# Kernel optimization log

Measured on AMD Instinct MI355X. Metric: run time of the kernel, lower is better.

## Reference

```python
import jax, jax.numpy as jnp
import numpy as np

B, L, H, E = 4, 2048, 8, 64
S, D = L, E  # causal mask forces L == S


def setup_inputs() -> dict:
    key = jax.random.key(0)
    kq, kk, kv, km = jax.random.split(key, 4)
    return {
        "queries": jax.random.normal(kq, (B, L, H, E), dtype=jnp.float32),
        "keys": jax.random.normal(kk, (B, S, H, E), dtype=jnp.float32),
        "values": jax.random.normal(kv, (B, S, H, D), dtype=jnp.float32),
        "map": jax.random.normal(km, (S, S), dtype=jnp.float32),
    }


def reference(queries, keys, values, map):
    # queries: [B,L,H,E], keys: [B,S,H,E], values: [B,S,H,D], map: [S,S]
    E_ = queries.shape[-1]
    scale = 1.0 / jnp.sqrt(jnp.asarray(E_, dtype=queries.dtype))
    # raw attention scores: [B,H,L,S]
    scores = jnp.einsum("blhe,bshe->bhls", queries, keys)
    # mix scores with learned map along the key axis: [B,H,L,S]
    scores = jnp.einsum("bhls,st->bhlt", scores, map)
    # causal mask (TriangularCausalMask: triu with diagonal=1 is masked)
    Lq = queries.shape[1]
    causal = jnp.triu(jnp.ones((Lq, Lq), dtype=bool), k=1)  # [L,S]
    scores = jnp.where(causal[None, None, :, :], -jnp.inf, scores)
    attn = jax.nn.softmax(scale * scores, axis=-1)  # dropout p=0.0 -> identity
    out = jnp.einsum("bhls,bshd->blhd", attn, values)  # [B,L,H,D]
    return out
```

## Files before the change

kernel.cpp:

```cpp
#include <hip/hip_runtime.h>


typedef short bf16x8 __attribute__((ext_vector_type(8)));
typedef float f32x4 __attribute__((ext_vector_type(4)));
typedef float f32x16 __attribute__((ext_vector_type(16)));
typedef unsigned short u16x8 __attribute__((ext_vector_type(8)));
typedef unsigned int u32x4 __attribute__((ext_vector_type(4)));

typedef __attribute__((address_space(1))) const void gvoid;
typedef __attribute__((address_space(3))) void lvoid;

__device__ __forceinline__ unsigned short f2bf(float x) {
  unsigned int u = __float_as_uint(x);
  u += 0x7FFFu + ((u >> 16) & 1u);
  return (unsigned short)(u >> 16);
}
__device__ __forceinline__ float bf2f(unsigned short h) {
  return __uint_as_float(((unsigned int)h) << 16);
}
__device__ __forceinline__ unsigned int cvtpk(float lo, float hi) {
  unsigned int r;
  asm("v_cvt_pk_bf16_f32 %0, %1, %2" : "=v"(r) : "v"(lo), "v"(hi));
  return r;
}

__device__ __forceinline__ void gload16(const unsigned short* g, unsigned short* l) {
  __builtin_amdgcn_global_load_lds((gvoid*)g, (lvoid*)l, 16, 0, 0);
}

template <int NW>
__device__ __forceinline__ void stage_tile(const unsigned short* __restrict__ g,
                                           int gstride, unsigned short* l,
                                           int rows, int tid) {
  const int lane = tid & 63, w = tid >> 6;
  const int nch = rows << 3;
  for (int c0 = (w << 6); c0 < nch; c0 += NW * 64) {
    const int c = c0 + lane;
    const int row = c >> 3;
    const int bir = (c & 7) << 4;
    const int sb = bir ^ ((row & 7) << 4);
    gload16(g + (size_t)row * gstride + (sb >> 1), l + (size_t)c0 * 8);
  }
}

__device__ __forceinline__ int swz(int row, int byteInRow) {
  return row * 128 + (byteInRow ^ ((row & 7) << 4));
}

__global__ __launch_bounds__(256) void prep_m(const float* __restrict__ M,
                                              unsigned short* __restrict__ Mh,
                                              unsigned short* __restrict__ Ml) {
  __shared__ float Ts[64][68];
  const int s0 = blockIdx.x << 6, t0 = blockIdx.y << 6;
  const int tid = threadIdx.x, r = tid >> 2, c0 = (tid & 3) << 4;
  const float* src = M + (size_t)(s0 + r) * 2048 + t0 + c0;
#pragma unroll
  for (int j = 0; j < 4; ++j)
    *(float4*)&Ts[r][c0 + 4 * j] = *(const float4*)(src + 4 * j);
  __syncthreads();
  u16x8 h0, h1, l0v, l1v;
#pragma unroll
  for (int j = 0; j < 8; ++j) {
    float x = Ts[c0 + j][r];
    unsigned short hh = f2bf(x);
    h0[j] = hh; l0v[j] = f2bf(x - bf2f(hh));
  }
#pragma unroll
  for (int j = 8; j < 16; ++j) {
    float x = Ts[c0 + j][r];
    unsigned short hh = f2bf(x);
    h1[j - 8] = hh; l1v[j - 8] = f2bf(x - bf2f(hh));
  }
  const size_t o = (size_t)(t0 + r) * 2048 + s0 + c0;
  *(u16x8*)(Mh + o) = h0; *(u16x8*)(Mh + o + 8) = h1;
  *(u16x8*)(Ml + o) = l0v; *(u16x8*)(Ml + o + 8) = l1v;
}

__global__ __launch_bounds__(256) void prep_kv(const float* __restrict__ src4d,
                                               unsigned short* __restrict__ Dh,
                                               unsigned short* __restrict__ Dl,
                                               int has_lo) {
  __shared__ float Ts[64][68];
  const int s0 = blockIdx.x << 6, bh = blockIdx.y;
  const int b = bh >> 3, h = bh & 7;
  const int tid = threadIdx.x, r = tid >> 2, c0 = (tid & 3) << 4;
  const float* src = src4d + ((size_t)(b * 2048 + s0 + r) * 8 + h) * 64 + c0;
#pragma unroll
  for (int j = 0; j < 4; ++j)
    *(float4*)&Ts[r][c0 + 4 * j] = *(const float4*)(src + 4 * j);
  __syncthreads();
  u16x8 h0, h1, l0v, l1v;
#pragma unroll
  for (int j = 0; j < 8; ++j) {
    float x = Ts[c0 + j][r];
    unsigned short hh = f2bf(x);
    h0[j] = hh; l0v[j] = f2bf(x - bf2f(hh));
  }
#pragma unroll
  for (int j = 8; j < 16; ++j) {
    float x = Ts[c0 + j][r];
    unsigned short hh = f2bf(x);
    h1[j - 8] = hh; l1v[j - 8] = f2bf(x - bf2f(hh));
  }
  const size_t o = ((size_t)bh * 64 + r) * 2048 + s0 + c0;
  *(u16x8*)(Dh + o) = h0; *(u16x8*)(Dh + o + 8) = h1;
  if (has_lo) { *(u16x8*)(Dl + o) = l0v; *(u16x8*)(Dl + o + 8) = l1v; }
}

__global__ __launch_bounds__(256) void km_mfma(
    const unsigned short* __restrict__ Mth, const unsigned short* __restrict__ Mtl,
    const unsigned short* __restrict__ Kth, const unsigned short* __restrict__ Ktl,
    unsigned short* __restrict__ KMh, unsigned short* __restrict__ KMl) {
  __shared__ __attribute__((aligned(16))) unsigned short sm[24576];
  unsigned short* MtH = sm;
  unsigned short* MtL = sm + 8192;
  unsigned short* KtH = sm + 16384;
  unsigned short* KtL = sm + 20480;
  const int tid = threadIdx.x, lane = tid & 63, w = tid >> 6;
  const int g = lane >> 4, li = lane & 15;
  const int t0 = blockIdx.x << 7;
  const int bh = blockIdx.y;
  const unsigned short* KtHb = Kth + (size_t)bh * 64 * 2048;
  const unsigned short* KtLb = Ktl + (size_t)bh * 64 * 2048;

  f32x4 acc[2][4];
#pragma unroll
  for (int mi = 0; mi < 2; ++mi)
#pragma unroll
    for (int ni = 0; ni < 4; ++ni) acc[mi][ni] = (f32x4){0.f, 0.f, 0.f, 0.f};

  for (int s0 = 0; s0 < 2048; s0 += 64) {
    __syncthreads();
    stage_tile<4>(Mth + (size_t)t0 * 2048 + s0, 2048, MtH, 128, tid);
    stage_tile<4>(Mtl + (size_t)t0 * 2048 + s0, 2048, MtL, 128, tid);
    stage_tile<4>(KtHb + s0, 2048, KtH, 64, tid);
    stage_tile<4>(KtLb + s0, 2048, KtL, 64, tid);
    asm volatile("s_waitcnt vmcnt(0)" ::: "memory");
    __syncthreads();
#pragma unroll
    for (int kk = 0; kk < 2; ++kk) {
      const int kb = (kk * 32 + 8 * g) * 2;
      bf16x8 aH[2], aL[2];
#pragma unroll
      for (int mi = 0; mi < 2; ++mi) {
        const int row = (w << 5) + (mi << 4) + li;
        aH[mi] = *(const bf16x8*)((const char*)MtH + swz(row, kb));
        aL[mi] = *(const bf16x8*)((const char*)MtL + swz(row, kb));
      }
#pragma unroll
      for (int ni = 0; ni < 4; ++ni) {
        const int row = (ni << 4) + li;
        const int off = swz(row, kb);
        const bf16x8 bH = *(const bf16x8*)((const char*)KtH + off);
        const bf16x8 bL = *(const bf16x8*)((const char*)KtL + off);
#pragma unroll
        for (int mi = 0; mi < 2; ++mi) {
          acc[mi][ni] = __builtin_amdgcn_mfma_f32_16x16x32_bf16(aH[mi], bH, acc[mi][ni], 0, 0, 0);
          acc[mi][ni] = __builtin_amdgcn_mfma_f32_16x16x32_bf16(aH[mi], bL, acc[mi][ni], 0, 0, 0);
          acc[mi][ni] = __builtin_amdgcn_mfma_f32_16x16x32_bf16(aL[mi], bH, acc[mi][ni], 0, 0, 0);
        }
      }
    }
  }
  const size_t base = (size_t)bh * 2048 * 64;
#pragma unroll
  for (int mi = 0; mi < 2; ++mi)
#pragma unroll
    for (int r = 0; r < 4; ++r) {
      const int trow = t0 + (w << 5) + (mi << 4) + (g << 2) + r;
#pragma unroll
      for (int ni = 0; ni < 4; ++ni) {
        const float x = acc[mi][ni][r];
        const unsigned short hh = f2bf(x);
        const size_t idx = base + (size_t)trow * 64 + (ni << 4) + li;
        KMh[idx] = hh;
        KMl[idx] = f2bf(x - bf2f(hh));
      }
    }
}

__global__ __launch_bounds__(256, 3) void attn32(
    const float* __restrict__ Q, const unsigned short* __restrict__ KMh,
    const unsigned short* __restrict__ KMl, const unsigned short* __restrict__ Vt,
    float* __restrict__ Out, float* __restrict__ Opart, float* __restrict__ Ml) {
  __shared__ __attribute__((aligned(16))) unsigned short sm[24576];
  const int tid = threadIdx.x, lane = tid & 63, w = tid >> 6;
  const int g2 = lane >> 5, li5 = lane & 31;

  const int bid = (int)blockIdx.x;
  const int x = bid & 7, n = bid >> 3;
  const int slot = n >> 5, j = n & 31;
  const int bh = (x << 2) | (j & 3);
  const int kk = j >> 2;
  int lt, jt0, jtEnd;
  bool partial;
  if (slot == 2) {
    lt = kk; jt0 = 0; jtEnd = 2 * kk + 1; partial = false;
  } else {
    lt = 15 - kk;
    const int half = 16 - kk;
    jt0 = slot * half; jtEnd = jt0 + half - 1; partial = true;
  }
  const int b = bh >> 3, h = bh & 7;
  const int l0 = lt << 7;
  const int qg = l0 + (w << 5) + li5;
  const int rloc = (w << 5) + li5;

  const float SC2 = 0.18033688011112042f;
  bf16x8 qh[4], ql[4];
  {
    const float* qsrc = Q + (((size_t)(b * 2048 + qg) * 8 + h) << 6) + (g2 << 3);
#pragma unroll
    for (int kki = 0; kki < 4; ++kki) {
      const float4 v0 = *(const float4*)(qsrc + 16 * kki);
      const float4 v1 = *(const float4*)(qsrc + 16 * kki + 4);
      const float xs[8] = {v0.x, v0.y, v0.z, v0.w, v1.x, v1.y, v1.z, v1.w};
#pragma unroll
      for (int jj = 0; jj < 8; ++jj) {
        const float xv = xs[jj] * SC2;
        const unsigned short hh = f2bf(xv);
        qh[kki][jj] = (short)hh;
        ql[kki][jj] = (short)f2bf(xv - bf2f(hh));
      }
    }
  }

  f32x16 o0 = {0,0,0,0,0,0,0,0,0,0,0,0,0,0,0,0};
  f32x16 o1 = {0,0,0,0,0,0,0,0,0,0,0,0,0,0,0,0};
  f32x16 lsacc = {0,0,0,0,0,0,0,0,0,0,0,0,0,0,0,0};
  float m2 = -1e30f;
  bf16x8 ones;
#pragma unroll
  for (int jj = 0; jj < 8; ++jj) ones[jj] = (short)0x3F80;

  const unsigned short* KHb = KMh + (size_t)bh * 2048 * 64;
  const unsigned short* KLb = KMl + (size_t)bh * 2048 * 64;
  const unsigned short* VTb = Vt + (size_t)bh * 64 * 2048;

  const int jtmax_w = 2 * lt + (w >> 1);

  {
    unsigned short* s0b = sm + (jt0 & 1) * 12288;
    stage_tile<4>(KHb + (size_t)jt0 * 4096, 64, s0b, 64, tid);
    stage_tile<4>(KLb + (size_t)jt0 * 4096, 64, s0b + 4096, 64, tid);
    stage_tile<4>(VTb + jt0 * 64, 2048, s0b + 8192, 64, tid);
  }
  asm volatile("s_waitcnt vmcnt(0)" ::: "memory");
  __builtin_amdgcn_s_barrier();
  __builtin_amdgcn_sched_barrier(0);

  for (int jt = jt0; jt <= jtEnd; ++jt) {
    const int cur = jt & 1;
    if (jt < jtEnd) {
      unsigned short* nb = sm + (cur ^ 1) * 12288;
      stage_tile<4>(KHb + (size_t)(jt + 1) * 4096, 64, nb, 64, tid);
      stage_tile<4>(KLb + (size_t)(jt + 1) * 4096, 64, nb + 4096, 64, tid);
      stage_tile<4>(VTb + (jt + 1) * 64, 2048, nb + 8192, 64, tid);
    }

    if (jt <= jtmax_w) {
      const unsigned short* KH = sm + cur * 12288;
      const unsigned short* KL = KH + 4096;
      const unsigned short* VT = KH + 8192;

      f32x16 z0 = {0,0,0,0,0,0,0,0,0,0,0,0,0,0,0,0};
      f32x16 z1 = {0,0,0,0,0,0,0,0,0,0,0,0,0,0,0,0};
      __builtin_amdgcn_s_setprio(1);
#pragma unroll
      for (int kki = 0; kki < 4; ++kki) {
        const int cb = 32 * kki + 16 * g2;
        const bf16x8 a0h = *(const bf16x8*)((const char*)KH + swz(li5, cb));
        const bf16x8 a0l = *(const bf16x8*)((const char*)KL + swz(li5, cb));
        const bf16x8 a1h = *(const bf16x8*)((const char*)KH + swz(32 + li5, cb));
        const bf16x8 a1l = *(const bf16x8*)((const char*)KL + swz(32 + li5, cb));
        z0 = __builtin_amdgcn_mfma_f32_32x32x16_bf16(a0h, qh[kki], z0, 0, 0, 0);
        z0 = __builtin_amdgcn_mfma_f32_32x32x16_bf16(a0h, ql[kki], z0, 0, 0, 0);
        z0 = __builtin_amdgcn_mfma_f32_32x32x16_bf16(a0l, qh[kki], z0, 0, 0, 0);
        z1 = __builtin_amdgcn_mfma_f32_32x32x16_bf16(a1h, qh[kki], z1, 0, 0, 0);
        z1 = __builtin_amdgcn_mfma_f32_32x32x16_bf16(a1h, ql[kki], z1, 0, 0, 0);
        z1 = __builtin_amdgcn_mfma_f32_32x32x16_bf16(a1l, qh[kki], z1, 0, 0, 0);
      }
      __builtin_amdgcn_s_setprio(0);

      const bool needmask = (jt * 64 + 63 > l0 + (w << 5));
      if (needmask) {
        const int thr = qg - jt * 64;
#pragma unroll
        for (int rr = 0; rr < 16; ++rr) {
          const int tl = (g2 << 2) + ((rr >> 2) << 3) + (rr & 3);
          if (tl > thr) z0[rr] = -1e30f;
          if (tl + 32 > thr) z1[rr] = -1e30f;
        }
      }

      float t16[16];
#pragma unroll
      for (int rr = 0; rr < 16; ++rr) t16[rr] = fmaxf(z0[rr], z1[rr]);
#pragma unroll
      for (int s = 8; s; s >>= 1)
#pragma unroll
        for (int rr = 0; rr < 8; ++rr)
          if (rr < s) t16[rr] = fmaxf(t16[rr], t16[rr + s]);
      const float mx = fmaxf(t16[0], __shfl_xor(t16[0], 32));
      if (__any(mx > m2 + 11.0f)) {
        const float m2n = fmaxf(m2, mx);
        const float fs = exp2f(m2 - m2n);
        m2 = m2n;
#pragma unroll
        for (int rr = 0; rr < 16; ++rr) { o0[rr] *= fs; o1[rr] *= fs; }
        lsacc[0] *= fs;
      }

      float pv0[16], pv1[16];
#pragma unroll
      for (int rr = 0; rr < 16; ++rr) {
        pv0[rr] = exp2f(z0[rr] - m2);
        pv1[rr] = exp2f(z1[rr] - m2);
      }
      unsigned int W0[8], W1[8];
#pragma unroll
      for (int i = 0; i < 8; ++i) {
        W0[i] = cvtpk(pv0[2 * i], pv0[2 * i + 1]);
        W1[i] = cvtpk(pv1[2 * i], pv1[2 * i + 1]);
      }
      asm volatile("v_permlane32_swap_b32 %0, %1" : "+v"(W0[0]), "+v"(W0[2]));
      asm volatile("v_permlane32_swap_b32 %0, %1" : "+v"(W0[1]), "+v"(W0[3]));
      asm volatile("v_permlane32_swap_b32 %0, %1" : "+v"(W0[4]), "+v"(W0[6]));
      asm volatile("v_permlane32_swap_b32 %0, %1" : "+v"(W0[5]), "+v"(W0[7]));
      asm volatile("v_permlane32_swap_b32 %0, %1" : "+v"(W1[0]), "+v"(W1[2]));
      asm volatile("v_permlane32_swap_b32 %0, %1" : "+v"(W1[1]), "+v"(W1[3]));
      asm volatile("v_permlane32_swap_b32 %0, %1" : "+v"(W1[4]), "+v"(W1[6]));
      asm volatile("v_permlane32_swap_b32 %0, %1" : "+v"(W1[5]), "+v"(W1[7]));
      bf16x8 pf[4];
      {
        u32x4 f0 = {W0[0], W0[1], W0[2], W0[3]};
        u32x4 f1 = {W0[4], W0[5], W0[6], W0[7]};
        u32x4 f2 = {W1[0], W1[1], W1[2], W1[3]};
        u32x4 f3 = {W1[4], W1[5], W1[6], W1[7]};
        pf[0] = __builtin_bit_cast(bf16x8, f0);
        pf[1] = __builtin_bit_cast(bf16x8, f1);
        pf[2] = __builtin_bit_cast(bf16x8, f2);
        pf[3] = __builtin_bit_cast(bf16x8, f3);
      }

      __builtin_amdgcn_s_setprio(1);
#pragma unroll
      for (int kki = 0; kki < 4; ++kki) {
        const int cb = 32 * kki + 16 * g2;
        const bf16x8 v0f = *(const bf16x8*)((const char*)VT + swz(li5, cb));
        const bf16x8 v1f = *(const bf16x8*)((const char*)VT + swz(32 + li5, cb));
        o0 = __builtin_amdgcn_mfma_f32_32x32x16_bf16(v0f, pf[kki], o0, 0, 0, 0);
        o1 = __builtin_amdgcn_mfma_f32_32x32x16_bf16(v1f, pf[kki], o1, 0, 0, 0);
        lsacc = __builtin_amdgcn_mfma_f32_32x32x16_bf16(ones, pf[kki], lsacc, 0, 0, 0);
      }
      __builtin_amdgcn_s_setprio(0);
    }

    asm volatile("s_waitcnt vmcnt(0)" ::: "memory");
    __builtin_amdgcn_s_barrier();
    __builtin_amdgcn_sched_barrier(0);
  }

  if (!partial) {
    const float inv = 1.f / lsacc[0];
    float* ob = Out + (((size_t)(b * 2048 + qg) * 8 + h) << 6);
#pragma unroll
    for (int r2 = 0; r2 < 4; ++r2) {
      const int doff = (g2 << 2) + (r2 << 3);
      float4 s0 = make_float4(o0[4 * r2] * inv, o0[4 * r2 + 1] * inv,
                              o0[4 * r2 + 2] * inv, o0[4 * r2 + 3] * inv);
      *(float4*)(ob + doff) = s0;
      float4 s1 = make_float4(o1[4 * r2] * inv, o1[4 * r2 + 1] * inv,
                              o1[4 * r2 + 2] * inv, o1[4 * r2 + 3] * inv);
      *(float4*)(ob + 32 + doff) = s1;
    }
  } else {
    const size_t pidx = (((size_t)slot * 32 + bh) * 8 + kk) * 128 + rloc;
    float* op = Opart + pidx * 64;
#pragma unroll
    for (int r2 = 0; r2 < 4; ++r2) {
      const int doff = (g2 << 2) + (r2 << 3);
      *(float4*)(op + doff) =
          make_float4(o0[4 * r2], o0[4 * r2 + 1], o0[4 * r2 + 2], o0[4 * r2 + 3]);
      *(float4*)(op + 32 + doff) =
          make_float4(o1[4 * r2], o1[4 * r2 + 1], o1[4 * r2 + 2], o1[4 * r2 + 3]);
    }
    Ml[pidx * 2] = m2;
    Ml[pidx * 2 + 1] = lsacc[0];
  }
}

__global__ __launch_bounds__(256) void attn_combine(
    const float* __restrict__ Opart, const float* __restrict__ Ml,
    float* __restrict__ Out) {
  const int tid = threadIdx.x;
  const int rowg = (int)blockIdx.x * 32 + (tid >> 3);
  const int d0 = (tid & 7) << 3;
  const int r = rowg & 127, kk = (rowg >> 7) & 7, bh = rowg >> 10;
  const int b = bh >> 3, h = bh & 7;
  const int lt = 15 - kk;
  const size_t pidx = (((size_t)bh * 8 + kk) * 128 + r);
  const size_t PSLOT = (size_t)32 * 8 * 128 * 64;
  const size_t MSLOT = (size_t)32 * 8 * 128 * 2;
  const float m0 = Ml[pidx * 2], ls0 = Ml[pidx * 2 + 1];
  const float m1 = Ml[MSLOT + pidx * 2], ls1 = Ml[MSLOT + pidx * 2 + 1];
  const float mm = fmaxf(m0, m1);
  const float w0 = exp2f(m0 - mm), w1 = exp2f(m1 - mm);
  const float inv = 1.f / (ls0 * w0 + ls1 * w1);
  const float* p0 = Opart + pidx * 64 + d0;
  const float* p1 = Opart + PSLOT + pidx * 64 + d0;
  const float4 a0 = *(const float4*)(p0);
  const float4 a1 = *(const float4*)(p0 + 4);
  const float4 b0 = *(const float4*)(p1);
  const float4 b1 = *(const float4*)(p1 + 4);
  const int qg = lt * 128 + r;
  float* o = Out + (((size_t)(b * 2048 + qg) * 8 + h) << 6) + d0;
  *(float4*)o = make_float4((a0.x * w0 + b0.x * w1) * inv,
                            (a0.y * w0 + b0.y * w1) * inv,
                            (a0.z * w0 + b0.z * w1) * inv,
                            (a0.w * w0 + b0.w * w1) * inv);
  *(float4*)(o + 4) = make_float4((a1.x * w0 + b1.x * w1) * inv,
                                  (a1.y * w0 + b1.y * w1) * inv,
                                  (a1.z * w0 + b1.z * w1) * inv,
                                  (a1.w * w0 + b1.w * w1) * inv);
}

extern "C" void kernel_launch(void* const* d_in, const int* in_sizes, int n_in,
                              void* d_out, int out_size, void* d_ws, size_t ws_size,
                              hipStream_t stream) {
  const float* Q = (const float*)d_in[0];
  const float* K = (const float*)d_in[1];
  const float* V = (const float*)d_in[2];
  const float* M = (const float*)d_in[3];
  float* Out = (float*)d_out;
  char* ws = (char*)d_ws;
  const size_t MB = 1u << 20;
  unsigned short* Mth = (unsigned short*)(ws);
  unsigned short* Mtl = (unsigned short*)(ws + 8 * MB);
  unsigned short* Kth = (unsigned short*)(ws + 16 * MB);
  unsigned short* Ktl = (unsigned short*)(ws + 24 * MB);
  unsigned short* Vts = (unsigned short*)(ws + 32 * MB);
  unsigned short* KMh = (unsigned short*)(ws + 40 * MB);
  unsigned short* KMl = (unsigned short*)(ws + 48 * MB);
  float* Opart = (float*)(ws);
  float* Mlp = (float*)(ws + 16 * MB);

  prep_m<<<dim3(32, 32), 256, 0, stream>>>(M, Mth, Mtl);
  prep_kv<<<dim3(32, 32), 256, 0, stream>>>(K, Kth, Ktl, 1);
  prep_kv<<<dim3(32, 32), 256, 0, stream>>>(V, Vts, (unsigned short*)nullptr, 0);
  km_mfma<<<dim3(16, 32), 256, 0, stream>>>(Mth, Mtl, Kth, Ktl, KMh, KMl);
  attn32<<<dim3(768), 256, 0, stream>>>(Q, KMh, KMl, Vts, Out, Opart, Mlp);
  attn_combine<<<dim3(1024), 256, 0, stream>>>(Opart, Mlp, Out);
}
```

Before: 147.9 us.

## Split every query tile in half, single-buffer V, store bf16 partials

Every query tile's key range is now split into two halves across 1024 blocks, replacing the mixed full and partial scheme. All outputs then go through the combine kernel, and the partials are stored as bf16 instead of fp32. V staging uses a single LDS buffer loaded each iteration, with a mid-iteration barrier and vmcnt wait, while K hi/lo stay double-buffered. This shrinks LDS so four blocks fit per CU. The aim is better load balance and occupancy and less partial-output traffic. The cost is an extra barrier per tile, combine work for every row, and bf16 rounding of the partial accumulators.

```diff
diff --git a/kernel.cpp b/kernel.cpp
--- a/kernel.cpp
+++ b/kernel.cpp
@@ -45,6 +45,10 @@
 
 __device__ __forceinline__ int swz(int row, int byteInRow) {
   return row * 128 + (byteInRow ^ ((row & 7) << 4));
+}
+
+__device__ __forceinline__ int chunk_off(int c, int gstride) {
+  return (c >> 3) * gstride + ((((c & 7) ^ ((c >> 3) & 7))) << 3);
 }
 
 __global__ __launch_bounds__(256) void prep_m(const float* __restrict__ M,
@@ -179,11 +183,11 @@
     }
 }
 
-__global__ __launch_bounds__(256, 3) void attn32(
+__global__ __launch_bounds__(256, 4) void attn32(
     const float* __restrict__ Q, const unsigned short* __restrict__ KMh,
     const unsigned short* __restrict__ KMl, const unsigned short* __restrict__ Vt,
-    float* __restrict__ Out, float* __restrict__ Opart, float* __restrict__ Ml) {
-  __shared__ __attribute__((aligned(16))) unsigned short sm[24576];
+    unsigned short* __restrict__ Opart, float* __restrict__ Ml) {
+  __shared__ __attribute__((aligned(16))) unsigned short sm[20480];
   const int tid = threadIdx.x, lane = tid & 63, w = tid >> 6;
   const int g2 = lane >> 5, li5 = lane & 31;
 
@@ -191,20 +195,22 @@
   const int x = bid & 7, n = bid >> 3;
   const int slot = n >> 5, j = n & 31;
   const int bh = (x << 2) | (j & 3);
-  const int kk = j >> 2;
-  int lt, jt0, jtEnd;
-  bool partial;
-  if (slot == 2) {
-    lt = kk; jt0 = 0; jtEnd = 2 * kk + 1; partial = false;
-  } else {
-    lt = 15 - kk;
-    const int half = 16 - kk;
-    jt0 = slot * half; jtEnd = jt0 + half - 1; partial = true;
-  }
+  const int k = j >> 2;
+  const int hf = slot & 1;
+  const int lt = (slot < 2) ? (15 - k) : k;
+  const int half = lt + 1;
+  const int jt0 = hf * half;
+  const int jtEnd = jt0 + half - 1;
   const int b = bh >> 3, h = bh & 7;
   const int l0 = lt << 7;
   const int qg = l0 + (w << 5) + li5;
   const int rloc = (w << 5) + li5;
+
+  const int c0 = tid, c1 = tid + 256;
+  const int ko0 = chunk_off(c0, 64), ko1 = chunk_off(c1, 64);
+  const int vo0 = chunk_off(c0, 2048), vo1 = chunk_off(c1, 2048);
+  const int ld0 = c0 << 3, ld1 = c1 << 3;
+  unsigned short* VTl = sm + 16384;
 
   const float SC2 = 0.18033688011112042f;
   bf16x8 qh[4], ql[4];
@@ -233,35 +239,41 @@
 #pragma unroll
   for (int jj = 0; jj < 8; ++jj) ones[jj] = (short)0x3F80;
 
-  const unsigned short* KHb = KMh + (size_t)bh * 2048 * 64;
-  const unsigned short* KLb = KMl + (size_t)bh * 2048 * 64;
-  const unsigned short* VTb = Vt + (size_t)bh * 64 * 2048;
+  const unsigned short* khsrc = KMh + (size_t)bh * 2048 * 64 + (size_t)jt0 * 4096;
+  const unsigned short* klsrc = KMl + (size_t)bh * 2048 * 64 + (size_t)jt0 * 4096;
+  const unsigned short* vsrc = Vt + (size_t)bh * 64 * 2048 + jt0 * 64;
 
   const int jtmax_w = 2 * lt + (w >> 1);
 
   {
-    unsigned short* s0b = sm + (jt0 & 1) * 12288;
-    stage_tile<4>(KHb + (size_t)jt0 * 4096, 64, s0b, 64, tid);
-    stage_tile<4>(KLb + (size_t)jt0 * 4096, 64, s0b + 4096, 64, tid);
-    stage_tile<4>(VTb + jt0 * 64, 2048, s0b + 8192, 64, tid);
-  }
+    unsigned short* kb = sm + ((jt0 & 1) << 13);
+    gload16(khsrc + ko0, kb + ld0);
+    gload16(khsrc + ko1, kb + ld1);
+    gload16(klsrc + ko0, kb + 4096 + ld0);
+    gload16(klsrc + ko1, kb + 4096 + ld1);
+  }
+  khsrc += 4096; klsrc += 4096;
   asm volatile("s_waitcnt vmcnt(0)" ::: "memory");
   __builtin_amdgcn_s_barrier();
   __builtin_amdgcn_sched_barrier(0);
 
   for (int jt = jt0; jt <= jtEnd; ++jt) {
-    const int cur = jt & 1;
-    if (jt < jtEnd) {
-      unsigned short* nb = sm + (cur ^ 1) * 12288;
-      stage_tile<4>(KHb + (size_t)(jt + 1) * 4096, 64, nb, 64, tid);
-      stage_tile<4>(KLb + (size_t)(jt + 1) * 4096, 64, nb + 4096, 64, tid);
-      stage_tile<4>(VTb + (jt + 1) * 64, 2048, nb + 8192, 64, tid);
-    }
-
-    if (jt <= jtmax_w) {
-      const unsigned short* KH = sm + cur * 12288;
+    gload16(vsrc + vo0, VTl + ld0);
+    gload16(vsrc + vo1, VTl + ld1);
+    {
+      unsigned short* kb = sm + (((jt + 1) & 1) << 13);
+      gload16(khsrc + ko0, kb + ld0);
+      gload16(khsrc + ko1, kb + ld1);
+      gload16(klsrc + ko0, kb + 4096 + ld0);
+      gload16(klsrc + ko1, kb + 4096 + ld1);
+    }
+    khsrc += 4096; klsrc += 4096; vsrc += 64;
+
+    const bool act = (jt <= jtmax_w);
+    bf16x8 pf[4];
+    if (act) {
+      const unsigned short* KH = sm + ((jt & 1) << 13);
       const unsigned short* KL = KH + 4096;
-      const unsigned short* VT = KH + 8192;
 
       f32x16 z0 = {0,0,0,0,0,0,0,0,0,0,0,0,0,0,0,0};
       f32x16 z1 = {0,0,0,0,0,0,0,0,0,0,0,0,0,0,0,0};
@@ -331,7 +343,6 @@
       asm volatile("v_permlane32_swap_b32 %0, %1" : "+v"(W1[1]), "+v"(W1[3]));
       asm volatile("v_permlane32_swap_b32 %0, %1" : "+v"(W1[4]), "+v"(W1[6]));
       asm volatile("v_permlane32_swap_b32 %0, %1" : "+v"(W1[5]), "+v"(W1[7]));
-      bf16x8 pf[4];
       {
         u32x4 f0 = {W0[0], W0[1], W0[2], W0[3]};
         u32x4 f1 = {W0[4], W0[5], W0[6], W0[7]};
@@ -342,13 +353,19 @@
         pf[2] = __builtin_bit_cast(bf16x8, f2);
         pf[3] = __builtin_bit_cast(bf16x8, f3);
       }
-
+    }
+
+    asm volatile("s_waitcnt vmcnt(4)" ::: "memory");
+    __builtin_amdgcn_s_barrier();
+    __builtin_amdgcn_sched_barrier(0);
+
+    if (act) {
       __builtin_amdgcn_s_setprio(1);
 #pragma unroll
       for (int kki = 0; kki < 4; ++kki) {
         const int cb = 32 * kki + 16 * g2;
-        const bf16x8 v0f = *(const bf16x8*)((const char*)VT + swz(li5, cb));
-        const bf16x8 v1f = *(const bf16x8*)((const char*)VT + swz(32 + li5, cb));
+        const bf16x8 v0f = *(const bf16x8*)((const char*)VTl + swz(li5, cb));
+        const bf16x8 v1f = *(const bf16x8*)((const char*)VTl + swz(32 + li5, cb));
         o0 = __builtin_amdgcn_mfma_f32_32x32x16_bf16(v0f, pf[kki], o0, 0, 0, 0);
         o1 = __builtin_amdgcn_mfma_f32_32x32x16_bf16(v1f, pf[kki], o1, 0, 0, 0);
         lsacc = __builtin_amdgcn_mfma_f32_32x32x16_bf16(ones, pf[kki], lsacc, 0, 0, 0);
@@ -361,68 +378,52 @@
     __builtin_amdgcn_sched_barrier(0);
   }
 
-  if (!partial) {
-    const float inv = 1.f / lsacc[0];
-    float* ob = Out + (((size_t)(b * 2048 + qg) * 8 + h) << 6);
-#pragma unroll
-    for (int r2 = 0; r2 < 4; ++r2) {
-      const int doff = (g2 << 2) + (r2 << 3);
-      float4 s0 = make_float4(o0[4 * r2] * inv, o0[4 * r2 + 1] * inv,
-                              o0[4 * r2 + 2] * inv, o0[4 * r2 + 3] * inv);
-      *(float4*)(ob + doff) = s0;
-      float4 s1 = make_float4(o1[4 * r2] * inv, o1[4 * r2 + 1] * inv,
-                              o1[4 * r2 + 2] * inv, o1[4 * r2 + 3] * inv);
-      *(float4*)(ob + 32 + doff) = s1;
-    }
-  } else {
-    const size_t pidx = (((size_t)slot * 32 + bh) * 8 + kk) * 128 + rloc;
-    float* op = Opart + pidx * 64;
-#pragma unroll
-    for (int r2 = 0; r2 < 4; ++r2) {
-      const int doff = (g2 << 2) + (r2 << 3);
-      *(float4*)(op + doff) =
-          make_float4(o0[4 * r2], o0[4 * r2 + 1], o0[4 * r2 + 2], o0[4 * r2 + 3]);
-      *(float4*)(op + 32 + doff) =
-          make_float4(o1[4 * r2], o1[4 * r2 + 1], o1[4 * r2 + 2], o1[4 * r2 + 3]);
-    }
-    Ml[pidx * 2] = m2;
-    Ml[pidx * 2 + 1] = lsacc[0];
-  }
+  const size_t pidx = (((size_t)bh * 16 + lt) << 7) + rloc;
+  unsigned short* op = Opart + (size_t)hf * 4194304 + pidx * 64;
+#pragma unroll
+  for (int r2 = 0; r2 < 4; ++r2) {
+    const int doff = (g2 << 2) + (r2 << 3);
+    uint2 pa, pb;
+    pa.x = cvtpk(o0[4 * r2], o0[4 * r2 + 1]);
+    pa.y = cvtpk(o0[4 * r2 + 2], o0[4 * r2 + 3]);
+    *(uint2*)(op + doff) = pa;
+    pb.x = cvtpk(o1[4 * r2], o1[4 * r2 + 1]);
+    pb.y = cvtpk(o1[4 * r2 + 2], o1[4 * r2 + 3]);
+    *(uint2*)(op + 32 + doff) = pb;
+  }
+  float* mlp = Ml + (((size_t)hf * 65536) + pidx) * 2;
+  mlp[0] = m2;
+  mlp[1] = lsacc[0];
 }
 
 __global__ __launch_bounds__(256) void attn_combine(
-    const float* __restrict__ Opart, const float* __restrict__ Ml,
+    const unsigned short* __restrict__ Opart, const float* __restrict__ Ml,
     float* __restrict__ Out) {
   const int tid = threadIdx.x;
   const int rowg = (int)blockIdx.x * 32 + (tid >> 3);
   const int d0 = (tid & 7) << 3;
-  const int r = rowg & 127, kk = (rowg >> 7) & 7, bh = rowg >> 10;
+  const int r = rowg & 127;
+  const int lt = (rowg >> 7) & 15;
+  const int bh = rowg >> 11;
   const int b = bh >> 3, h = bh & 7;
-  const int lt = 15 - kk;
-  const size_t pidx = (((size_t)bh * 8 + kk) * 128 + r);
-  const size_t PSLOT = (size_t)32 * 8 * 128 * 64;
-  const size_t MSLOT = (size_t)32 * 8 * 128 * 2;
+  const size_t pidx = (((size_t)bh * 16 + lt) << 7) + r;
+  const size_t HOFF = 4194304;
+  const size_t MOFF = 131072;
   const float m0 = Ml[pidx * 2], ls0 = Ml[pidx * 2 + 1];
-  const float m1 = Ml[MSLOT + pidx * 2], ls1 = Ml[MSLOT + pidx * 2 + 1];
+  const float m1 = Ml[MOFF + pidx * 2], ls1 = Ml[MOFF + pidx * 2 + 1];
   const float mm = fmaxf(m0, m1);
   const float w0 = exp2f(m0 - mm), w1 = exp2f(m1 - mm);
   const float inv = 1.f / (ls0 * w0 + ls1 * w1);
-  const float* p0 = Opart + pidx * 64 + d0;
-  const float* p1 = Opart + PSLOT + pidx * 64 + d0;
-  const float4 a0 = *(const float4*)(p0);
-  const float4 a1 = *(const float4*)(p0 + 4);
-  const float4 b0 = *(const float4*)(p1);
-  const float4 b1 = *(const float4*)(p1 + 4);
-  const int qg = lt * 128 + r;
+  const u16x8 A = *(const u16x8*)(Opart + pidx * 64 + d0);
+  const u16x8 Bv = *(const u16x8*)(Opart + HOFF + pidx * 64 + d0);
+  float res[8];
+#pragma unroll
+  for (int jj = 0; jj < 8; ++jj)
+    res[jj] = (bf2f(A[jj]) * w0 + bf2f(Bv[jj]) * w1) * inv;
+  const int qg = (lt << 7) + r;
   float* o = Out + (((size_t)(b * 2048 + qg) * 8 + h) << 6) + d0;
-  *(float4*)o = make_float4((a0.x * w0 + b0.x * w1) * inv,
-                            (a0.y * w0 + b0.y * w1) * inv,
-                            (a0.z * w0 + b0.z * w1) * inv,
-                            (a0.w * w0 + b0.w * w1) * inv);
-  *(float4*)(o + 4) = make_float4((a1.x * w0 + b1.x * w1) * inv,
-                                  (a1.y * w0 + b1.y * w1) * inv,
-                                  (a1.z * w0 + b1.z * w1) * inv,
-                                  (a1.w * w0 + b1.w * w1) * inv);
+  *(float4*)o = make_float4(res[0], res[1], res[2], res[3]);
+  *(float4*)(o + 4) = make_float4(res[4], res[5], res[6], res[7]);
 }
 
 extern "C" void kernel_launch(void* const* d_in, const int* in_sizes, int n_in,
@@ -442,13 +443,13 @@
   unsigned short* Vts = (unsigned short*)(ws + 32 * MB);
   unsigned short* KMh = (unsigned short*)(ws + 40 * MB);
   unsigned short* KMl = (unsigned short*)(ws + 48 * MB);
-  float* Opart = (float*)(ws);
+  unsigned short* Opart = (unsigned short*)(ws);
   float* Mlp = (float*)(ws + 16 * MB);
 
   prep_m<<<dim3(32, 32), 256, 0, stream>>>(M, Mth, Mtl);
   prep_kv<<<dim3(32, 32), 256, 0, stream>>>(K, Kth, Ktl, 1);
   prep_kv<<<dim3(32, 32), 256, 0, stream>>>(V, Vts, (unsigned short*)nullptr, 0);
   km_mfma<<<dim3(16, 32), 256, 0, stream>>>(Mth, Mtl, Kth, Ktl, KMh, KMl);
-  attn32<<<dim3(768), 256, 0, stream>>>(Q, KMh, KMl, Vts, Out, Opart, Mlp);
-  attn_combine<<<dim3(1024), 256, 0, stream>>>(Opart, Mlp, Out);
-}
+  attn32<<<dim3(1024), 256, 0, stream>>>(Q, KMh, KMl, Vts, Opart, Mlp);
+  attn_combine<<<dim3(2048), 256, 0, stream>>>(Opart, Mlp, Out);
+}
```

New measurement: 169.2 us. +14.4%, slower.
